# Optimization experiments

Measured on AMD Instinct MI355X. Metric: run time of the kernel, lower is better.

The kernel has to match this reference:

```python
import jax, jax.numpy as jnp
import numpy as np

N_NODES = 200000
INPUT_DIM = 128
HIDDEN_DIM = 128
NUM_WALKS = 16384   # total walks across the batch of graphs
WALK_LEN = 20


def setup_inputs() -> dict:
    key = jax.random.key(0)
    ks = jax.random.split(key, 6)
    s_in = 1.0 / np.sqrt(INPUT_DIM)
    s_h = 1.0 / np.sqrt(HIDDEN_DIM)
    return {
        "x": jax.random.normal(ks[0], (N_NODES, INPUT_DIM), dtype=jnp.float32),
        "walks": jax.random.randint(ks[1], (NUM_WALKS, WALK_LEN), 0, N_NODES),
        "W_f": jax.random.normal(ks[2], (HIDDEN_DIM, INPUT_DIM), dtype=jnp.float32) * s_in,
        "b_f": jnp.zeros((HIDDEN_DIM,), dtype=jnp.float32),
        "W_ih": jax.random.normal(ks[3], (3 * HIDDEN_DIM, HIDDEN_DIM), dtype=jnp.float32) * s_h,
        "W_hh": jax.random.normal(ks[4], (3 * HIDDEN_DIM, HIDDEN_DIM), dtype=jnp.float32) * s_h,
        "b_ih": jnp.zeros((3 * HIDDEN_DIM,), dtype=jnp.float32),
        "b_hh": jnp.zeros((3 * HIDDEN_DIM,), dtype=jnp.float32),
    }


def _gru_final(seq, W_ih, W_hh, b_ih, b_hh):
    # seq: [B, T, H]; torch GRU gate order: reset, update, new. Returns final h: [B, H].
    B = seq.shape[0]
    H = W_hh.shape[1]

    def step(h, x_t):
        gx = x_t @ W_ih.T + b_ih            # [B, 3H]
        gh = h @ W_hh.T + b_hh              # [B, 3H]
        xr, xz, xn = jnp.split(gx, 3, axis=-1)
        hr, hz, hn = jnp.split(gh, 3, axis=-1)
        r = jax.nn.sigmoid(xr + hr)
        z = jax.nn.sigmoid(xz + hz)
        n = jnp.tanh(xn + r * hn)
        h_new = (1.0 - z) * n + z * h
        return h_new, None

    h0 = jnp.zeros((B, H), dtype=seq.dtype)
    h_final, _ = jax.lax.scan(step, h0, jnp.swapaxes(seq, 0, 1))  # scan over time
    return h_final


def reference(x, walks, W_f, b_f, W_ih, W_hh, b_ih, b_hh):
    # feature_encoder: Linear(input_dim -> hidden_dim)
    x_encoded = x @ W_f.T + b_f             # [N, H]
    # vectorized replacement of the scalar double-loop gather
    walk_features = x_encoded[walks]        # [B, T, H]
    path_encodings = _gru_final(walk_features, W_ih, W_hh, b_ih, b_hh)  # [B, H]
    return path_encodings
```

## Files before the change

### kernel.cpp

```cpp
#include <hip/hip_runtime.h>
#include <cstddef>

#define NWALKS 16384
#define TLEN   20
#define HDIM   128
#define WPB    32
#define NTHR   512
#define HSTR   136

typedef __attribute__((ext_vector_type(8))) _Float16 f16x8;
typedef __attribute__((ext_vector_type(4))) _Float16 f16x4;
typedef __attribute__((ext_vector_type(2))) __fp16   h16x2;
typedef __attribute__((ext_vector_type(4))) float    f32x4;

union H4 { f16x4 v; struct { h16x2 lo, hi; } p; };

__global__ void fold_kernel(const float* __restrict__ W_f, const float* __restrict__ b_f,
                            const float* __restrict__ W_ih, const float* __restrict__ W_hh,
                            const float* __restrict__ b_ih,
                            _Float16* __restrict__ Wc16, _Float16* __restrict__ Whh16,
                            float* __restrict__ b_c) {
  const int r = blockIdx.x;
  const int i = threadIdx.x;
  const float* wih = W_ih + r * HDIM;
  float acc = 0.f;
  for (int h = 0; h < HDIM; ++h) acc = fmaf(wih[h], W_f[h * HDIM + i], acc);
  Wc16[r * HDIM + i]  = (_Float16)acc;
  Whh16[r * HDIM + i] = (_Float16)W_hh[r * HDIM + i];
  if (i == 0) {
    float bb = b_ih[r];
    for (int h = 0; h < HDIM; ++h) bb = fmaf(wih[h], b_f[h], bb);
    b_c[r] = bb;
  }
}

__device__ __forceinline__ float fsig(float v) {
  return __builtin_amdgcn_rcpf(1.f + __builtin_amdgcn_exp2f(-1.4426950408889634f * v));
}
__device__ __forceinline__ float ftanh(float v) {
  const float e2 = __builtin_amdgcn_exp2f(2.8853900817779268f * v);
  return fmaf(-2.f, __builtin_amdgcn_rcpf(e2 + 1.f), 1.f);
}

__global__ __launch_bounds__(NTHR, 2)
void gru_kernel(const float* __restrict__ x, const int* __restrict__ walks,
                const _Float16* __restrict__ Wc16, const _Float16* __restrict__ Whh16,
                const float* __restrict__ b_c, const float* __restrict__ b_hh,
                float* __restrict__ out) {
  __shared__ _Float16 hbuf[2][WPB][HSTR];
  __shared__ _Float16 xbuf[2][WPB][HSTR];
  __shared__ int      nodes[TLEN][WPB];

  const int tid  = threadIdx.x;
  const int lane = tid & 63;
  const int wv   = tid >> 6;
  const int g    = lane >> 4;
  const int l15  = lane & 15;
  const int jw   = wv * 16 + l15;
  const int j0   = wv * 16 + 4 * g;
  const int walk0 = blockIdx.x * WPB;

  for (int idx = tid; idx < TLEN * WPB; idx += NTHR)
    nodes[idx >> 5][idx & 31] = walks[(walk0 + (idx & 31)) * TLEN + (idx >> 5)];
  for (int idx = tid; idx < WPB * HDIM; idx += NTHR)
    hbuf[0][idx >> 7][idx & 127] = (_Float16)0.f;

  f16x8 wrx[4], wrh[4], wzx[4], wzh[4], wnx[4], wnh[4];
#pragma unroll
  for (int kt = 0; kt < 4; ++kt) {
    const int koff = kt * 32 + g * 8;
    wrx[kt] = *(const f16x8*)(Wc16  + (size_t)(jw)       * HDIM + koff);
    wzx[kt] = *(const f16x8*)(Wc16  + (size_t)(128 + jw) * HDIM + koff);
    wnx[kt] = *(const f16x8*)(Wc16  + (size_t)(256 + jw) * HDIM + koff);
    wrh[kt] = *(const f16x8*)(Whh16 + (size_t)(jw)       * HDIM + koff);
    wzh[kt] = *(const f16x8*)(Whh16 + (size_t)(128 + jw) * HDIM + koff);
    wnh[kt] = *(const f16x8*)(Whh16 + (size_t)(256 + jw) * HDIM + koff);
  }
  const f32x4 br4  = *(const f32x4*)&b_c[j0]        + *(const f32x4*)&b_hh[j0];
  const f32x4 bz4  = *(const f32x4*)&b_c[128 + j0]  + *(const f32x4*)&b_hh[128 + j0];
  const f32x4 bxn4 = *(const f32x4*)&b_c[256 + j0];
  const f32x4 bhn4 = *(const f32x4*)&b_hh[256 + j0];

  f32x4 hprev[2];
  hprev[0] = 0.f; hprev[1] = 0.f;

  const int srow = tid >> 4;
  const int sc   = tid & 15;

  __syncthreads();

  {
    const unsigned off0 = ((unsigned)nodes[0][srow] << 7) + sc * 8u;
    const f32x4 a = *(const f32x4*)(x + off0);
    const f32x4 b = *(const f32x4*)(x + off0 + 4);
    H4 lo, hi;
    lo.p.lo = __builtin_amdgcn_cvt_pkrtz(a.x, a.y);
    lo.p.hi = __builtin_amdgcn_cvt_pkrtz(a.z, a.w);
    hi.p.lo = __builtin_amdgcn_cvt_pkrtz(b.x, b.y);
    hi.p.hi = __builtin_amdgcn_cvt_pkrtz(b.z, b.w);
    *(f16x4*)&xbuf[0][srow][sc * 8]     = lo.v;
    *(f16x4*)&xbuf[0][srow][sc * 8 + 4] = hi.v;
  }
  f32x4 PA0, PA1, PB0, PB1;
  {
    const unsigned off1 = ((unsigned)nodes[1][srow] << 7) + sc * 8u;
    PA0 = *(const f32x4*)(x + off1);
    PA1 = *(const f32x4*)(x + off1 + 4);
  }
  __syncthreads();

#define STEP(T, CUR, NXT, P0, P1, N0, N1)                                         \
  {                                                                               \
                             \
    const int tn = ((T) + 2 < TLEN) ? (T) + 2 : TLEN - 1;                         \
    const unsigned offn = ((unsigned)nodes[tn][srow] << 7) + sc * 8u;             \
    N0 = *(const f32x4*)(x + offn);                                               \
    N1 = *(const f32x4*)(x + offn + 4);                                           \
                                         \
    f32x4 ar[2], az[2], an[2], ah2[2];                                            \
    ar[0] = br4;  ar[1] = br4;  az[0] = bz4;  az[1] = bz4;                        \
    an[0] = bxn4; an[1] = bxn4; ah2[0] = bhn4; ah2[1] = bhn4;                     \
    _Pragma("unroll")                                                             \
    for (int kt = 0; kt < 4; ++kt) {                                              \
      const int koff = kt * 32 + g * 8;                                           \
      const f16x8 ax0 = *(const f16x8*)&xbuf[CUR][l15][koff];                     \
      const f16x8 ax1 = *(const f16x8*)&xbuf[CUR][16 + l15][koff];                \
      const f16x8 ah0 = *(const f16x8*)&hbuf[CUR][l15][koff];                     \
      const f16x8 ah1 = *(const f16x8*)&hbuf[CUR][16 + l15][koff];                \
      ar[0]  = __builtin_amdgcn_mfma_f32_16x16x32_f16(wrx[kt], ax0, ar[0],  0,0,0); \
      ar[1]  = __builtin_amdgcn_mfma_f32_16x16x32_f16(wrx[kt], ax1, ar[1],  0,0,0); \
      ar[0]  = __builtin_amdgcn_mfma_f32_16x16x32_f16(wrh[kt], ah0, ar[0],  0,0,0); \
      ar[1]  = __builtin_amdgcn_mfma_f32_16x16x32_f16(wrh[kt], ah1, ar[1],  0,0,0); \
      az[0]  = __builtin_amdgcn_mfma_f32_16x16x32_f16(wzx[kt], ax0, az[0],  0,0,0); \
      az[1]  = __builtin_amdgcn_mfma_f32_16x16x32_f16(wzx[kt], ax1, az[1],  0,0,0); \
      az[0]  = __builtin_amdgcn_mfma_f32_16x16x32_f16(wzh[kt], ah0, az[0],  0,0,0); \
      az[1]  = __builtin_amdgcn_mfma_f32_16x16x32_f16(wzh[kt], ah1, az[1],  0,0,0); \
      an[0]  = __builtin_amdgcn_mfma_f32_16x16x32_f16(wnx[kt], ax0, an[0],  0,0,0); \
      an[1]  = __builtin_amdgcn_mfma_f32_16x16x32_f16(wnx[kt], ax1, an[1],  0,0,0); \
      ah2[0] = __builtin_amdgcn_mfma_f32_16x16x32_f16(wnh[kt], ah0, ah2[0], 0,0,0); \
      ah2[1] = __builtin_amdgcn_mfma_f32_16x16x32_f16(wnh[kt], ah1, ah2[1], 0,0,0); \
    }                                                                             \
                    \
    {                                                                             \
      H4 lo, hi;                                                                  \
      lo.p.lo = __builtin_amdgcn_cvt_pkrtz(P0.x, P0.y);                           \
      lo.p.hi = __builtin_amdgcn_cvt_pkrtz(P0.z, P0.w);                           \
      hi.p.lo = __builtin_amdgcn_cvt_pkrtz(P1.x, P1.y);                           \
      hi.p.hi = __builtin_amdgcn_cvt_pkrtz(P1.z, P1.w);                           \
      *(f16x4*)&xbuf[NXT][srow][sc * 8]     = lo.v;                               \
      *(f16x4*)&xbuf[NXT][srow][sc * 8 + 4] = hi.v;                               \
    }                                                                             \
                                   \
    _Pragma("unroll")                                                             \
    for (int mt = 0; mt < 2; ++mt) {                                              \
      f32x4 hn;                                                                   \
      _Pragma("unroll")                                                           \
      for (int r = 0; r < 4; ++r) {                                               \
        const float rv = fsig(ar[mt][r]);                                         \
        const float zv = fsig(az[mt][r]);                                         \
        const float nv = ftanh(fmaf(rv, ah2[mt][r], an[mt][r]));                  \
        hn[r] = fmaf(zv, hprev[mt][r] - nv, nv);                                  \
      }                                                                           \
      hprev[mt] = hn;                                                             \
      H4 hp;                                                                      \
      hp.p.lo = __builtin_amdgcn_cvt_pkrtz(hn[0], hn[1]);                         \
      hp.p.hi = __builtin_amdgcn_cvt_pkrtz(hn[2], hn[3]);                         \
      *(f16x4*)&hbuf[NXT][mt * 16 + l15][j0] = hp.v;                              \
    }                                                                             \
    __syncthreads();                                                              \
  }

#pragma unroll 1
  for (int tt = 0; tt < TLEN; tt += 2) {
    STEP(tt,     0, 1, PA0, PA1, PB0, PB1)
    STEP(tt + 1, 1, 0, PB0, PB1, PA0, PA1)
  }
#undef STEP

#pragma unroll
  for (int mt = 0; mt < 2; ++mt) {
    float4 o = make_float4(hprev[mt][0], hprev[mt][1], hprev[mt][2], hprev[mt][3]);
    *(float4*)&out[(size_t)(walk0 + mt * 16 + l15) * HDIM + j0] = o;
  }
}

extern "C" void kernel_launch(void* const* d_in, const int* in_sizes, int n_in,
                              void* d_out, int out_size, void* d_ws, size_t ws_size,
                              hipStream_t stream) {
  const float* x     = (const float*)d_in[0];
  const int*   walks = (const int*)  d_in[1];
  const float* W_f   = (const float*)d_in[2];
  const float* b_f   = (const float*)d_in[3];
  const float* W_ih  = (const float*)d_in[4];
  const float* W_hh  = (const float*)d_in[5];
  const float* b_ih  = (const float*)d_in[6];
  const float* b_hh  = (const float*)d_in[7];
  float* out = (float*)d_out;

  _Float16* Wc16  = (_Float16*)d_ws;
  _Float16* Whh16 = Wc16 + 384 * HDIM;
  float*    b_c   = (float*)(Whh16 + 384 * HDIM);

  fold_kernel<<<3 * HDIM, HDIM, 0, stream>>>(W_f, b_f, W_ih, W_hh, b_ih, Wc16, Whh16, b_c);
  gru_kernel<<<NWALKS / WPB, NTHR, 0, stream>>>(x, walks, Wc16, Whh16, b_c, b_hh, out);
}
```

Baseline: 85.24 us.

## Swizzle LDS layout, fold activation scales into weights, seed MFMA accumulators with bias

Replaces the padded LDS rows with an XOR-swizzled layout for the x and h staging buffers, to avoid bank conflicts without padding. Folds the sigmoid and tanh exp2 scale factors into the fp16 weights and biases in the fold kernel, which removes per-element multiplies from the gate math. Bias vectors now seed the first MFMA accumulator directly instead of being copied in. s_setprio is raised around the MFMA block. Scaling the weights before the fp16 cast slightly changes rounding and range.

```diff
diff --git a/kernel.cpp b/kernel.cpp
--- a/kernel.cpp
+++ b/kernel.cpp
@@ -6,7 +6,6 @@
 #define HDIM   128
 #define WPB    32
 #define NTHR   512
-#define HSTR   136
 
 typedef __attribute__((ext_vector_type(8))) _Float16 f16x8;
 typedef __attribute__((ext_vector_type(4))) _Float16 f16x4;
@@ -22,24 +21,17 @@
                             float* __restrict__ b_c) {
   const int r = blockIdx.x;
   const int i = threadIdx.x;
+  const float scale = (r < 256) ? -1.4426950408889634f : 2.8853900817779268f;
   const float* wih = W_ih + r * HDIM;
   float acc = 0.f;
   for (int h = 0; h < HDIM; ++h) acc = fmaf(wih[h], W_f[h * HDIM + i], acc);
-  Wc16[r * HDIM + i]  = (_Float16)acc;
-  Whh16[r * HDIM + i] = (_Float16)W_hh[r * HDIM + i];
+  Wc16[r * HDIM + i]  = (_Float16)(acc * scale);
+  Whh16[r * HDIM + i] = (_Float16)(W_hh[r * HDIM + i] * scale);
   if (i == 0) {
     float bb = b_ih[r];
     for (int h = 0; h < HDIM; ++h) bb = fmaf(wih[h], b_f[h], bb);
     b_c[r] = bb;
   }
-}
-
-__device__ __forceinline__ float fsig(float v) {
-  return __builtin_amdgcn_rcpf(1.f + __builtin_amdgcn_exp2f(-1.4426950408889634f * v));
-}
-__device__ __forceinline__ float ftanh(float v) {
-  const float e2 = __builtin_amdgcn_exp2f(2.8853900817779268f * v);
-  return fmaf(-2.f, __builtin_amdgcn_rcpf(e2 + 1.f), 1.f);
 }
 
 __global__ __launch_bounds__(NTHR, 2)
@@ -47,8 +39,8 @@
                 const _Float16* __restrict__ Wc16, const _Float16* __restrict__ Whh16,
                 const float* __restrict__ b_c, const float* __restrict__ b_hh,
                 float* __restrict__ out) {
-  __shared__ _Float16 hbuf[2][WPB][HSTR];
-  __shared__ _Float16 xbuf[2][WPB][HSTR];
+  __shared__ _Float16 hbuf[2][WPB][HDIM];
+  __shared__ _Float16 xbuf[2][WPB][HDIM];
   __shared__ int      nodes[TLEN][WPB];
 
   const int tid  = threadIdx.x;
@@ -63,7 +55,7 @@
   for (int idx = tid; idx < TLEN * WPB; idx += NTHR)
     nodes[idx >> 5][idx & 31] = walks[(walk0 + (idx & 31)) * TLEN + (idx >> 5)];
   for (int idx = tid; idx < WPB * HDIM; idx += NTHR)
-    hbuf[0][idx >> 7][idx & 127] = (_Float16)0.f;
+    hbuf[0][0][idx] = (_Float16)0.f;
 
   f16x8 wrx[4], wrh[4], wzx[4], wzh[4], wnx[4], wnh[4];
 #pragma unroll
@@ -76,16 +68,24 @@
     wzh[kt] = *(const f16x8*)(Whh16 + (size_t)(128 + jw) * HDIM + koff);
     wnh[kt] = *(const f16x8*)(Whh16 + (size_t)(256 + jw) * HDIM + koff);
   }
-  const f32x4 br4  = *(const f32x4*)&b_c[j0]        + *(const f32x4*)&b_hh[j0];
-  const f32x4 bz4  = *(const f32x4*)&b_c[128 + j0]  + *(const f32x4*)&b_hh[128 + j0];
-  const f32x4 bxn4 = *(const f32x4*)&b_c[256 + j0];
-  const f32x4 bhn4 = *(const f32x4*)&b_hh[256 + j0];
+  const float NEG_L2E = -1.4426950408889634f;
+  const float TWO_L2E =  2.8853900817779268f;
+  const f32x4 br4  = NEG_L2E * (*(const f32x4*)&b_c[j0]       + *(const f32x4*)&b_hh[j0]);
+  const f32x4 bz4  = NEG_L2E * (*(const f32x4*)&b_c[128 + j0] + *(const f32x4*)&b_hh[128 + j0]);
+  const f32x4 bxn4 = TWO_L2E * (*(const f32x4*)&b_c[256 + j0]);
+  const f32x4 bhn4 = TWO_L2E * (*(const f32x4*)&b_hh[256 + j0]);
 
   f32x4 hprev[2];
   hprev[0] = 0.f; hprev[1] = 0.f;
 
+  int voffs[4];
+#pragma unroll
+  for (int kt = 0; kt < 4; ++kt)
+    voffs[kt] = l15 * HDIM + ((((kt * 4 + g) ^ (l15 & 7))) << 3);
   const int srow = tid >> 4;
   const int sc   = tid & 15;
+  const int xw   = srow * HDIM + ((sc ^ (srow & 7)) << 3);
+  const int hw   = l15 * HDIM + (((2 * wv + (g >> 1)) ^ (l15 & 7)) << 3) + ((g & 1) << 2);
 
   __syncthreads();
 
@@ -98,8 +98,8 @@
     lo.p.hi = __builtin_amdgcn_cvt_pkrtz(a.z, a.w);
     hi.p.lo = __builtin_amdgcn_cvt_pkrtz(b.x, b.y);
     hi.p.hi = __builtin_amdgcn_cvt_pkrtz(b.z, b.w);
-    *(f16x4*)&xbuf[0][srow][sc * 8]     = lo.v;
-    *(f16x4*)&xbuf[0][srow][sc * 8 + 4] = hi.v;
+    *(f16x4*)(&xbuf[0][0][0] + xw)     = lo.v;
+    *(f16x4*)(&xbuf[0][0][0] + xw + 4) = hi.v;
   }
   f32x4 PA0, PA1, PB0, PB1;
   {
@@ -116,30 +116,31 @@
     const unsigned offn = ((unsigned)nodes[tn][srow] << 7) + sc * 8u;             \
     N0 = *(const f32x4*)(x + offn);                                               \
     N1 = *(const f32x4*)(x + offn + 4);                                           \
-                                         \
+                                      \
+    const _Float16* xb = &xbuf[CUR][0][0];                                        \
+    const _Float16* hb = &hbuf[CUR][0][0];                                        \
     f32x4 ar[2], az[2], an[2], ah2[2];                                            \
-    ar[0] = br4;  ar[1] = br4;  az[0] = bz4;  az[1] = bz4;                        \
-    an[0] = bxn4; an[1] = bxn4; ah2[0] = bhn4; ah2[1] = bhn4;                     \
+    __builtin_amdgcn_s_setprio(1);                                                \
     _Pragma("unroll")                                                             \
     for (int kt = 0; kt < 4; ++kt) {                                              \
-      const int koff = kt * 32 + g * 8;                                           \
-      const f16x8 ax0 = *(const f16x8*)&xbuf[CUR][l15][koff];                     \
-      const f16x8 ax1 = *(const f16x8*)&xbuf[CUR][16 + l15][koff];                \
-      const f16x8 ah0 = *(const f16x8*)&hbuf[CUR][l15][koff];                     \
-      const f16x8 ah1 = *(const f16x8*)&hbuf[CUR][16 + l15][koff];                \
-      ar[0]  = __builtin_amdgcn_mfma_f32_16x16x32_f16(wrx[kt], ax0, ar[0],  0,0,0); \
-      ar[1]  = __builtin_amdgcn_mfma_f32_16x16x32_f16(wrx[kt], ax1, ar[1],  0,0,0); \
+      const f16x8 ax0 = *(const f16x8*)(xb + voffs[kt]);                          \
+      const f16x8 ax1 = *(const f16x8*)(xb + voffs[kt] + 16 * HDIM);              \
+      const f16x8 ah0 = *(const f16x8*)(hb + voffs[kt]);                          \
+      const f16x8 ah1 = *(const f16x8*)(hb + voffs[kt] + 16 * HDIM);              \
+      ar[0]  = __builtin_amdgcn_mfma_f32_16x16x32_f16(wrx[kt], ax0, kt ? ar[0]  : br4,  0,0,0); \
+      ar[1]  = __builtin_amdgcn_mfma_f32_16x16x32_f16(wrx[kt], ax1, kt ? ar[1]  : br4,  0,0,0); \
       ar[0]  = __builtin_amdgcn_mfma_f32_16x16x32_f16(wrh[kt], ah0, ar[0],  0,0,0); \
       ar[1]  = __builtin_amdgcn_mfma_f32_16x16x32_f16(wrh[kt], ah1, ar[1],  0,0,0); \
-      az[0]  = __builtin_amdgcn_mfma_f32_16x16x32_f16(wzx[kt], ax0, az[0],  0,0,0); \
-      az[1]  = __builtin_amdgcn_mfma_f32_16x16x32_f16(wzx[kt], ax1, az[1],  0,0,0); \
+      az[0]  = __builtin_amdgcn_mfma_f32_16x16x32_f16(wzx[kt], ax0, kt ? az[0]  : bz4,  0,0,0); \
+      az[1]  = __builtin_amdgcn_mfma_f32_16x16x32_f16(wzx[kt], ax1, kt ? az[1]  : bz4,  0,0,0); \
       az[0]  = __builtin_amdgcn_mfma_f32_16x16x32_f16(wzh[kt], ah0, az[0],  0,0,0); \
       az[1]  = __builtin_amdgcn_mfma_f32_16x16x32_f16(wzh[kt], ah1, az[1],  0,0,0); \
-      an[0]  = __builtin_amdgcn_mfma_f32_16x16x32_f16(wnx[kt], ax0, an[0],  0,0,0); \
-      an[1]  = __builtin_amdgcn_mfma_f32_16x16x32_f16(wnx[kt], ax1, an[1],  0,0,0); \
-      ah2[0] = __builtin_amdgcn_mfma_f32_16x16x32_f16(wnh[kt], ah0, ah2[0], 0,0,0); \
-      ah2[1] = __builtin_amdgcn_mfma_f32_16x16x32_f16(wnh[kt], ah1, ah2[1], 0,0,0); \
+      an[0]  = __builtin_amdgcn_mfma_f32_16x16x32_f16(wnx[kt], ax0, kt ? an[0]  : bxn4, 0,0,0); \
+      an[1]  = __builtin_amdgcn_mfma_f32_16x16x32_f16(wnx[kt], ax1, kt ? an[1]  : bxn4, 0,0,0); \
+      ah2[0] = __builtin_amdgcn_mfma_f32_16x16x32_f16(wnh[kt], ah0, kt ? ah2[0] : bhn4, 0,0,0); \
+      ah2[1] = __builtin_amdgcn_mfma_f32_16x16x32_f16(wnh[kt], ah1, kt ? ah2[1] : bhn4, 0,0,0); \
     }                                                                             \
+    __builtin_amdgcn_s_setprio(0);                                                \
                     \
     {                                                                             \
       H4 lo, hi;                                                                  \
@@ -147,25 +148,26 @@
       lo.p.hi = __builtin_amdgcn_cvt_pkrtz(P0.z, P0.w);                           \
       hi.p.lo = __builtin_amdgcn_cvt_pkrtz(P1.x, P1.y);                           \
       hi.p.hi = __builtin_amdgcn_cvt_pkrtz(P1.z, P1.w);                           \
-      *(f16x4*)&xbuf[NXT][srow][sc * 8]     = lo.v;                               \
-      *(f16x4*)&xbuf[NXT][srow][sc * 8 + 4] = hi.v;                               \
+      *(f16x4*)(&xbuf[NXT][0][0] + xw)     = lo.v;                                \
+      *(f16x4*)(&xbuf[NXT][0][0] + xw + 4) = hi.v;                                \
     }                                                                             \
-                                   \
+                \
     _Pragma("unroll")                                                             \
     for (int mt = 0; mt < 2; ++mt) {                                              \
       f32x4 hn;                                                                   \
       _Pragma("unroll")                                                           \
       for (int r = 0; r < 4; ++r) {                                               \
-        const float rv = fsig(ar[mt][r]);                                         \
-        const float zv = fsig(az[mt][r]);                                         \
-        const float nv = ftanh(fmaf(rv, ah2[mt][r], an[mt][r]));                  \
+        const float rv = __builtin_amdgcn_rcpf(1.f + __builtin_amdgcn_exp2f(ar[mt][r])); \
+        const float zv = __builtin_amdgcn_rcpf(1.f + __builtin_amdgcn_exp2f(az[mt][r])); \
+        const float en = __builtin_amdgcn_exp2f(fmaf(rv, ah2[mt][r], an[mt][r])); \
+        const float nv = fmaf(-2.f, __builtin_amdgcn_rcpf(en + 1.f), 1.f);        \
         hn[r] = fmaf(zv, hprev[mt][r] - nv, nv);                                  \
       }                                                                           \
       hprev[mt] = hn;                                                             \
       H4 hp;                                                                      \
       hp.p.lo = __builtin_amdgcn_cvt_pkrtz(hn[0], hn[1]);                         \
       hp.p.hi = __builtin_amdgcn_cvt_pkrtz(hn[2], hn[3]);                         \
-      *(f16x4*)&hbuf[NXT][mt * 16 + l15][j0] = hp.v;                              \
+      *(f16x4*)(&hbuf[NXT][0][0] + hw + mt * 16 * HDIM) = hp.v;                   \
     }                                                                             \
     __syncthreads();                                                              \
   }
```

Measured after the change: 83.87 us. No clear change (-1.6%).
